# Optimization experiments

Measured on AMD Instinct MI355X. Metric: run time of the kernel, lower is better.

Reference implementation:

```python
import jax, jax.numpy as jnp
import numpy as np

T, N, D, V = 512, 256, 1024, 128000  # total tokens, sampled tokens, d_model, vocab


def setup_inputs() -> dict:
    key = jax.random.key(0)
    k1, k2, k3, k4, k5 = jax.random.split(key, 5)
    hidden_states = jax.random.normal(k1, (T, D), dtype=jnp.float32)
    embedding = jax.random.normal(k2, (V, D), dtype=jnp.float32) * 0.02
    # temperatures in [0.5, 1.5): realistic, avoids divide blow-up (0.0 maps to 1.0 in source)
    temperatures = 0.5 + jax.random.uniform(k3, (N,), dtype=jnp.float32)
    # top_p in [0.5, 1.0)
    top_ps = 0.5 + 0.5 * jax.random.uniform(k4, (N,), dtype=jnp.float32)
    last_token_indices = jnp.sort(jax.random.randint(k5, (N,), 0, T))
    return {
        "hidden_states": hidden_states,
        "embedding": embedding,
        "temperatures": temperatures,
        "top_ps": top_ps,
        "last_token_indices": last_token_indices,
    }


def reference(hidden_states, embedding, temperatures, top_ps, last_token_indices):
    # gather last-token hidden states, project to vocab logits
    h = hidden_states[last_token_indices]              # [N, D]
    logits = jnp.einsum("nd,vd->nv", h, embedding)     # [N, V]
    # temperature softmax
    probs = jax.nn.softmax(logits / temperatures[:, None], axis=-1)
    # top-p: descending sort, cumsum, mask tail, renormalize, un-sort
    order = jnp.argsort(-probs, axis=-1)               # descending order indices
    probs_sort = jnp.take_along_axis(probs, order, axis=-1)
    cum = jnp.cumsum(probs_sort, axis=-1)
    mask = (cum - probs_sort) > top_ps[:, None]
    probs_sort = jnp.where(mask, 0.0, probs_sort)
    probs_sort = probs_sort / jnp.sum(probs_sort, axis=-1, keepdims=True)
    inv = jnp.argsort(order, axis=-1)                  # inverse permutation
    probs_f = jnp.take_along_axis(probs_sort, inv, axis=-1)
    # multinomial sampling (one token per row), fixed key for determinism
    tokens = jax.random.categorical(jax.random.key(42), jnp.log(probs_f + 1e-20), axis=-1)
    return probs_f, tokens
```

## Files before the change

kernel.cpp:

```cpp
#include <hip/hip_runtime.h>
#include <stdint.h>

#define N_TOK 256
#define D_MODEL 1024
#define VOCAB 128000
#define NV_ELEMS (256LL * 128000LL)
#define LIST_CAP 24576
#define GLIST_CAP 16384

typedef unsigned long long u64;
typedef uint32_t u32;
typedef __attribute__((ext_vector_type(8))) short bfrag;
typedef __attribute__((ext_vector_type(4))) float facc;

__device__ __forceinline__ uint32_t bf16_rne_bits(float x) {
    uint32_t u = __float_as_uint(x);
    return (u + 0x7fffu + ((u >> 16) & 1u)) >> 16;
}

__device__ __forceinline__ uint32_t rotl32(uint32_t x, int d) {
    return (x << d) | (x >> (32 - d));
}

__device__ __forceinline__ u32 mono32(u32 b) {
    return (b & 0x80000000u) ? ~b : (b | 0x80000000u);
}
__device__ __forceinline__ float unmono32(u32 k) {
    u32 b = (k & 0x80000000u) ? (k & 0x7FFFFFFFu) : ~k;
    return __uint_as_float(b);
}

__device__ __forceinline__ u64 fixmass(float rv) {
    return (u64)(rv * 1073741824.0f);
}

__device__ __forceinline__ uint2 tf_0_42(uint32_t c0, uint32_t c1) {
    const uint32_t ks0 = 0u, ks1 = 42u, ks2 = 0x1BD11BDAu ^ 42u;
    uint32_t x0 = c0 + ks0, x1 = c1 + ks1;
#define R4(a,b,c,d) \
    x0 += x1; x1 = rotl32(x1,a); x1 ^= x0; \
    x0 += x1; x1 = rotl32(x1,b); x1 ^= x0; \
    x0 += x1; x1 = rotl32(x1,c); x1 ^= x0; \
    x0 += x1; x1 = rotl32(x1,d); x1 ^= x0;
    R4(13,15,26,6)   x0 += ks1; x1 += ks2 + 1u;
    R4(17,29,16,24)  x0 += ks2; x1 += ks0 + 2u;
    R4(13,15,26,6)   x0 += ks0; x1 += ks1 + 3u;
    R4(17,29,16,24)  x0 += ks1; x1 += ks2 + 4u;
    R4(13,15,26,6)   x0 += ks2; x1 += ks0 + 5u;
#undef R4
    return make_uint2(x0, x1);
}

__device__ __forceinline__ uint32_t jax_bits(uint32_t j) {
    uint2 r = tf_0_42(0u, j);
    return r.x ^ r.y;
}

__device__ __forceinline__ float jax_gumbel(uint32_t bits) {
    const float TINY = 1.17549435e-38f;
    float u = __uint_as_float((bits >> 9) | 0x3f800000u) - 1.0f;
    u = u + TINY;
    u = fmaxf(TINY, u);
    return -__logf(-__logf(u));
}

__device__ __forceinline__ float rv_of(float l, float rinv) {
    return __expf(l * rinv);
}

__device__ __forceinline__ void async_copy16(const void* g, void* lbase, int lane) {
#if defined(__has_builtin) && __has_builtin(__builtin_amdgcn_global_load_lds)
    __builtin_amdgcn_global_load_lds((const uint32_t*)g, (uint32_t*)lbase, 16, 0, 0);
#else
    *(bfrag*)((char*)lbase + lane * 16) = *(const bfrag*)g;
#endif
}

__device__ __forceinline__ void scan_desc_u64(const u64* h, int nb, u64 carry, u64 P,
                                              int* outCb, u64* outSa) {
    int lane = (int)threadIdx.x & 63;
    int chunk = nb >> 6;
    int top = nb - 1 - lane * chunk;
    u64 ls = 0ull;
    for (int j = 0; j < chunk; ++j) ls += h[top - j];
    u64 incl = ls;
    for (int o = 1; o < 64; o <<= 1) {
        u64 v = __shfl_up(incl, o, 64);
        if (lane >= o) incl += v;
    }
    u64 s0 = carry + incl - ls;
    unsigned long long mask = __ballot(s0 + ls > P);
    if (mask == 0ull) {
        if (lane == 0) { *outCb = 0; *outSa = carry; }
    } else {
        int cstar = (int)__builtin_ctzll(mask);
        if (lane == cstar) {
            u64 sa = s0; int cb = 0;
            for (int j = 0; j < chunk; ++j) {
                int b = top - j;
                if (sa + h[b] > P) { cb = b; break; }
                sa += h[b];
            }
            *outCb = cb; *outSa = sa;
        }
    }
}

__global__ __launch_bounds__(256) void prep_a(
        const float* __restrict__ hidden, const int* __restrict__ idx,
        ushort* __restrict__ wsA) {
    const int m = blockIdx.x;
    const int t = threadIdx.x;
    const float* src = hidden + (long long)idx[m] * D_MODEL;
    const uint32_t swz = (uint32_t)((m & 7) << 4);
    for (int j = 0; j < 4; ++j) {
        int k = t * 4 + j;
        float x = src[k];
        uint32_t hb = bf16_rne_bits(x);
        float hf = __uint_as_float(hb << 16);
        uint32_t lb = bf16_rne_bits(x - hf);
        int kt = k >> 5, kk = k & 31, g = kk >> 3, e = kk & 7;
        char* img = (char*)wsA + (size_t)kt * 32768;
        uint32_t base = (uint32_t)(m * 128 + g * 32);
        *(ushort*)(img + ((base + 0) ^ swz) + e * 2) = (ushort)hb;
        *(ushort*)(img + ((base + 16) ^ swz) + e * 2) = (ushort)lb;
    }
}

__global__ __launch_bounds__(256) void gemm_mfma(
        const ushort* __restrict__ wsA, const float* __restrict__ emb,
        float* __restrict__ logits) {
    __shared__ __align__(16) ushort Aimg[16384];
    __shared__ __align__(16) ushort Bimg[4096];
    const int tid = (int)threadIdx.x;
    const int w = tid >> 6, l = tid & 63;
    const int lr = l & 15, lg = l >> 4;
    const int v0 = blockIdx.x * 64;
    char* Ab = (char*)Aimg;
    char* Bb = (char*)Bimg;

    facc acc[4][4] = {};

    for (int kt = 0; kt < 32; ++kt) {
        __syncthreads();
        const char* asrc = (const char*)wsA + (size_t)kt * 32768;
#pragma unroll
        for (int i = 0; i < 8; ++i) {
            int off = w * 8192 + i * 1024;
            async_copy16(asrc + off + l * 16, Ab + off, l);
        }
        {
            int rb = tid >> 2, g = tid & 3;
            const float* bs = emb + (size_t)(v0 + rb) * D_MODEL + kt * 32 + g * 8;
            float4 x0 = *(const float4*)bs;
            float4 x1 = *(const float4*)(bs + 4);
            float xs[8] = {x0.x, x0.y, x0.z, x0.w, x1.x, x1.y, x1.z, x1.w};
            bfrag h, lo;
#pragma unroll
            for (int e = 0; e < 8; ++e) {
                uint32_t hb = bf16_rne_bits(xs[e]);
                float hf = __uint_as_float(hb << 16);
                uint32_t lb = bf16_rne_bits(xs[e] - hf);
                h[e] = (short)hb; lo[e] = (short)lb;
            }
            uint32_t swz = (uint32_t)((rb & 7) << 4);
            uint32_t base = (uint32_t)(rb * 128 + g * 32);
            *(bfrag*)(Bb + ((base + 0) ^ swz)) = h;
            *(bfrag*)(Bb + ((base + 16) ^ swz)) = lo;
        }
        __syncthreads();
        bfrag bh[4], bl[4];
#pragma unroll
        for (int nj = 0; nj < 4; ++nj) {
            int rb = nj * 16 + lr;
            uint32_t swz = (uint32_t)((rb & 7) << 4);
            uint32_t base = (uint32_t)(rb * 128 + lg * 32);
            bh[nj] = *(const bfrag*)(Bb + ((base + 0) ^ swz));
            bl[nj] = *(const bfrag*)(Bb + ((base + 16) ^ swz));
        }
#pragma unroll
        for (int mi = 0; mi < 4; ++mi) {
            int r = w * 64 + mi * 16 + lr;
            uint32_t swz = (uint32_t)((r & 7) << 4);
            uint32_t base = (uint32_t)(r * 128 + lg * 32);
            bfrag ah = *(const bfrag*)(Ab + ((base + 0) ^ swz));
            bfrag al = *(const bfrag*)(Ab + ((base + 16) ^ swz));
#pragma unroll
            for (int nj = 0; nj < 4; ++nj) {
                acc[mi][nj] = __builtin_amdgcn_mfma_f32_16x16x32_bf16(ah, bh[nj], acc[mi][nj], 0, 0, 0);
                acc[mi][nj] = __builtin_amdgcn_mfma_f32_16x16x32_bf16(ah, bl[nj], acc[mi][nj], 0, 0, 0);
                acc[mi][nj] = __builtin_amdgcn_mfma_f32_16x16x32_bf16(al, bh[nj], acc[mi][nj], 0, 0, 0);
            }
        }
    }
#pragma unroll
    for (int mi = 0; mi < 4; ++mi) {
        int mbase = w * 64 + mi * 16 + lg * 4;
#pragma unroll
        for (int nj = 0; nj < 4; ++nj) {
            int v = v0 + nj * 16 + lr;
#pragma unroll
            for (int reg = 0; reg < 4; ++reg)
                logits[(size_t)(mbase + reg) * VOCAB + v] = acc[mi][nj][reg];
        }
    }
}

__global__ __launch_bounds__(256) void gemm_kernel(
        const float* __restrict__ hidden, const int* __restrict__ idx,
        const float* __restrict__ emb, float* __restrict__ logits) {
    __shared__ float As[16][64];
    __shared__ float Bs[16][64];
    const int n0 = blockIdx.x * 64, v0 = blockIdx.y * 64;
    const int tid = threadIdx.x;
    const int tx = tid & 15, ty = tid >> 4;
    const int lr = tid >> 2, lk = (tid & 3) * 4;
    float acc[4][4] = {};
    const long long aRow = (long long)idx[n0 + lr] * D_MODEL + lk;
    const long long bRow = (long long)(v0 + lr) * D_MODEL + lk;
    for (int k0 = 0; k0 < D_MODEL; k0 += 16) {
        float4 av = *(const float4*)(hidden + aRow + k0);
        float4 bv = *(const float4*)(emb + bRow + k0);
        __syncthreads();
        As[lk + 0][lr] = av.x; As[lk + 1][lr] = av.y; As[lk + 2][lr] = av.z; As[lk + 3][lr] = av.w;
        Bs[lk + 0][lr] = bv.x; Bs[lk + 1][lr] = bv.y; Bs[lk + 2][lr] = bv.z; Bs[lk + 3][lr] = bv.w;
        __syncthreads();
#pragma unroll
        for (int kk = 0; kk < 16; ++kk) {
            float4 a = *(const float4*)&As[kk][ty * 4];
            float4 b = *(const float4*)&Bs[kk][tx * 4];
            float aa[4] = {a.x, a.y, a.z, a.w};
            float bb[4] = {b.x, b.y, b.z, b.w};
#pragma unroll
            for (int i = 0; i < 4; ++i)
#pragma unroll
                for (int j = 0; j < 4; ++j)
                    acc[i][j] += aa[i] * bb[j];
        }
    }
#pragma unroll
    for (int i = 0; i < 4; ++i) {
        float4 o = make_float4(acc[i][0], acc[i][1], acc[i][2], acc[i][3]);
        *(float4*)(logits + (long long)(n0 + ty * 4 + i) * VOCAB + (v0 + tx * 4)) = o;
    }
}

__global__ __launch_bounds__(512) void hist1_kernel(
        const float* __restrict__ probs, const float* __restrict__ temps,
        u64* __restrict__ ghist) {
    const int row = blockIdx.y, hb = blockIdx.x, tid = (int)threadIdx.x;
    __shared__ u64 h[4096];
    for (int i = tid; i < 4096; i += 512) h[i] = 0ull;
    __syncthreads();
    const float rinv = 1.0f / temps[row];
    const float4* R4 = (const float4*)(probs + (size_t)row * VOCAB);
    const int base4 = hb * 8000;
    for (int i = 0; i < 16; ++i) {
        int j = tid + i * 512;
        if (j < 8000) {
            float4 x = R4[base4 + j];
            float xs[4] = {x.x, x.y, x.z, x.w};
#pragma unroll
            for (int c = 0; c < 4; ++c) {
                u32 key = mono32(__float_as_uint(xs[c]));
                atomicAdd(&h[key >> 20], fixmass(rv_of(xs[c], rinv)));
            }
        }
    }
    __syncthreads();
    u64* gh = ghist + (size_t)row * 4096;
    for (int i = tid; i < 4096; i += 512)
        if (h[i]) atomicAdd(&gh[i], h[i]);
}

__global__ __launch_bounds__(64) void scan1_kernel(
        const u64* __restrict__ ghist, const float* __restrict__ topps,
        u64* __restrict__ rsP, u64* __restrict__ rsCarry, u32* __restrict__ rsCb) {
    const int row = blockIdx.x, lane = (int)threadIdx.x;
    const u64* h = ghist + (size_t)row * 4096;
    u64 S = 0ull;
    for (int j = lane; j < 4096; j += 64) S += h[j];
    for (int o = 32; o >= 1; o >>= 1) S += __shfl_xor(S, o, 64);
    const u64 P = (u64)((double)topps[row] * (double)S);
    __shared__ int sCb; __shared__ u64 sSa;
    scan_desc_u64(h, 4096, 0ull, P, &sCb, &sSa);
    __syncthreads();
    if (lane == 0) { rsP[row] = P; rsCarry[row] = sSa; rsCb[row] = (u32)sCb; }
}

__global__ __launch_bounds__(512) void compact_kernel(
        const float* __restrict__ probs, const u32* __restrict__ rsCb,
        u64* __restrict__ list, u32* __restrict__ listCnt) {
    const int row = blockIdx.y, hb = blockIdx.x, tid = (int)threadIdx.x;
    __shared__ u64 buf[4096];
    __shared__ u32 lcnt, gbase;
    const u32 cb1 = rsCb[row];
    const float4* R4 = (const float4*)(probs + (size_t)row * VOCAB);
    u64* lst = list + (size_t)row * GLIST_CAP;
    const int base4 = hb * 8000;
    if (tid == 0) lcnt = 0u;
    __syncthreads();
    for (int pair = 0; pair < 8; ++pair) {
#pragma unroll
        for (int s = 0; s < 2; ++s) {
            int j = tid + (pair * 2 + s) * 512;
            if (j < 8000) {
                float4 x = R4[base4 + j];
                float xs[4] = {x.x, x.y, x.z, x.w};
#pragma unroll
                for (int c = 0; c < 4; ++c) {
                    u32 key = mono32(__float_as_uint(xs[c]));
                    if ((key >> 20) == cb1) {
                        u32 pos = atomicAdd(&lcnt, 1u);
                        buf[pos] = ((u64)key << 32) | (u32)((base4 + j) * 4 + c);
                    }
                }
            }
        }
        __syncthreads();
        u32 n = lcnt;
        if (n) {
            if (tid == 0) gbase = atomicAdd(&listCnt[row], n);
            __syncthreads();
            u32 gb = gbase;
            for (u32 i2 = tid; i2 < n; i2 += 512) {
                u32 gpos = gb + i2;
                if (gpos < GLIST_CAP) lst[gpos] = buf[i2];
            }
        }
        __syncthreads();
        if (tid == 0) lcnt = 0u;
        __syncthreads();
    }
}

__global__ __launch_bounds__(1024) void resolve_kernel(
        const u64* __restrict__ list, const u32* __restrict__ listCnt,
        const u64* __restrict__ rsP, const u64* __restrict__ rsCarry,
        const u32* __restrict__ rsCb, const float* __restrict__ temps,
        u32* __restrict__ scTs, u32* __restrict__ scTieN,
        float* __restrict__ scInvSp, u32* __restrict__ tieKept) {
    const int row = blockIdx.x, tid = (int)threadIdx.x;
    __shared__ u64 h2[1024];
    __shared__ u32 c3[1024];
    __shared__ int sCb; __shared__ u64 sSa;
    __shared__ u32 sTc;
    __shared__ u32 tlist[1024];
    const u32 cnt = min(listCnt[row], (u32)GLIST_CAP);
    const u64 P = rsP[row];
    const float rinv = 1.0f / temps[row];
    const u64* lst = list + (size_t)row * GLIST_CAP;

    h2[tid] = 0ull;
    __syncthreads();
    for (u32 j = tid; j < cnt; j += 1024) {
        u32 key = (u32)(lst[j] >> 32);
        atomicAdd(&h2[(key >> 10) & 1023u], fixmass(rv_of(unmono32(key), rinv)));
    }
    __syncthreads();
    if (tid < 64) scan_desc_u64(h2, 1024, rsCarry[row], P, &sCb, &sSa);
    __syncthreads();
    const u32 cb2 = (u32)sCb; const u64 carry2 = sSa;
    __syncthreads();

    h2[tid] = 0ull; c3[tid] = 0u;
    __syncthreads();
    for (u32 j = tid; j < cnt; j += 1024) {
        u32 key = (u32)(lst[j] >> 32);
        if (((key >> 10) & 1023u) == cb2) {
            atomicAdd(&h2[key & 1023u], fixmass(rv_of(unmono32(key), rinv)));
            atomicAdd(&c3[key & 1023u], 1u);
        }
    }
    __syncthreads();
    if (tid < 64) scan_desc_u64(h2, 1024, carry2, P, &sCb, &sSa);
    __syncthreads();
    const int cb3 = sCb; const u64 sa3 = sSa;
    const u32 ts = (rsCb[row] << 20) | (cb2 << 10) | (u32)cb3;
    u32 cntb = c3[cb3]; if (cntb == 0u) cntb = 1u;
    const u64 tfq = fixmass(rv_of(unmono32(ts), rinv));
    const u64 rem = P - sa3;
    u32 mt;
    if (tfq == 0ull) mt = cntb;
    else {
        u64 q = rem / tfq;
        mt = (q >= (u64)(cntb - 1)) ? cntb : ((u32)q + 1u);
    }
    const u64 Spq = sa3 + (u64)mt * tfq;

    if (tid == 0) sTc = 0u;
    __syncthreads();
    for (u32 j = tid; j < cnt; j += 1024) {
        if ((u32)(lst[j] >> 32) == ts) {
            u32 pos = atomicAdd(&sTc, 1u);
            if (pos < 1024u) tlist[pos] = (u32)lst[j];
        }
    }
    __syncthreads();
    const u32 tn = min(sTc, 1024u);
    if ((u32)tid < tn) {
        u32 my = tlist[tid];
        u32 rank = 0;
        for (u32 j2 = 0; j2 < tn; ++j2) rank += (tlist[j2] < my) ? 1u : 0u;
        if (rank < mt) tieKept[(size_t)row * 1024 + rank] = my;
    }
    if (tid == 0) {
        scTs[row] = ts;
        scTieN[row] = min(mt, tn);
        scInvSp[row] = (float)(1073741824.0 / (double)Spq);
    }
}

__global__ __launch_bounds__(512) void final2_kernel(
        float* __restrict__ probs, const float* __restrict__ temps,
        const u32* __restrict__ scTs, const u32* __restrict__ scTieN,
        const float* __restrict__ scInvSp, const u32* __restrict__ tieKept,
        u64* __restrict__ argmax) {
    const int row = blockIdx.y, hb = blockIdx.x, tid = (int)threadIdx.x;
    __shared__ u32 tl[1024];
    __shared__ u64 wbest[8];
    const u32 ts = scTs[row], tieN = scTieN[row];
    const float invSp = scInvSp[row];
    const float rinv = 1.0f / temps[row];
    for (u32 i = tid; i < tieN; i += 512) tl[i] = tieKept[(size_t)row * 1024 + i];
    __syncthreads();
    float4* R4 = (float4*)(probs + (size_t)row * VOCAB);
    const u32 rowBase = (u32)row * (u32)VOCAB;
    const int base4 = hb * 8000;
    u64 best = 0ull;
    for (int i = 0; i < 16; ++i) {
        int j = tid + i * 512;
        if (j < 8000) {
            float4 x = R4[base4 + j];
            float xs[4] = {x.x, x.y, x.z, x.w};
            float4 out;
            float* op = (float*)&out;
#pragma unroll
            for (int c = 0; c < 4; ++c) {
                u32 key = mono32(__float_as_uint(xs[c]));
                u32 v = (u32)((base4 + j) * 4 + c);
                bool kept = key > ts;
                if (key == ts) {
                    kept = false;
                    for (u32 q2 = 0; q2 < tieN; ++q2)
                        if (tl[q2] == v) { kept = true; break; }
                }
                if (kept) {
                    float pf = rv_of(xs[c], rinv) * invSp;
                    op[c] = pf;
                    float g = jax_gumbel(jax_bits(rowBase + v));
                    float val = __logf(pf + 1e-20f) + g;
                    u64 pk = ((u64)mono32(__float_as_uint(val)) << 32) | (u32)(~v);
                    if (pk > best) best = pk;
                } else {
                    op[c] = 0.0f;
                }
            }
            R4[base4 + j] = out;
        }
    }
    for (int o = 32; o >= 1; o >>= 1) {
        u64 ob = __shfl_xor(best, o, 64);
        if (ob > best) best = ob;
    }
    if ((tid & 63) == 0) wbest[tid >> 6] = best;
    __syncthreads();
    if (tid == 0) {
        u64 b = wbest[0];
        for (int w2 = 1; w2 < 8; ++w2) if (wbest[w2] > b) b = wbest[w2];
        atomicMax(&argmax[row], b);
    }
}

__global__ void token_kernel(const u64* __restrict__ argmax, float* __restrict__ outTok) {
    int n = (int)threadIdx.x;
    if (n < N_TOK) outTok[n] = (float)(~(u32)argmax[n]);
}

__device__ __forceinline__ void scan_desc_wave(const float* h, int nb, float carry,
                                               float P, int* outCb, float* outSa) {
    int lane = (int)threadIdx.x & 63;
    int chunk = nb >> 6;
    int top = nb - 1 - lane * chunk;
    float ls = 0.0f;
    for (int j = 0; j < chunk; ++j) ls += h[top - j];
    float incl = ls;
    for (int o = 1; o < 64; o <<= 1) {
        float v = __shfl_up(incl, o, 64);
        if (lane >= o) incl += v;
    }
    float s0 = carry + incl - ls;
    unsigned long long mask = __ballot(s0 + ls > P);
    if (mask == 0ull) {
        if (lane == 63) { *outCb = 0; *outSa = carry + incl - h[0]; }
    } else {
        int cstar = (int)__builtin_ctzll(mask);
        if (lane == cstar) {
            float sa = s0; int cb = 0;
            for (int j = 0; j < chunk; ++j) {
                int b = top - j;
                if (sa + h[b] > P) { cb = b; break; }
                sa += h[b];
            }
            *outCb = cb; *outSa = sa;
        }
    }
}

__global__ __launch_bounds__(1024) void sample_kernel(
        float* __restrict__ probs, const float* __restrict__ temps,
        const float* __restrict__ topps, float* __restrict__ outTok) {
    const int row = blockIdx.x;
    const int tid = (int)threadIdx.x;
    float* L = probs + (long long)row * VOCAB;
    const float4* L4 = (const float4*)L;
    float4* L4w = (float4*)L;

    __shared__ float waveH[16][2048];
    __shared__ float hsum[2048];
    __shared__ uint32_t hcnt[1024];
    __shared__ float wred[16];
    __shared__ float aVal[16];
    __shared__ int aIdx[16];
    __shared__ uint32_t tieList[256];
    __shared__ int sCb;
    __shared__ float sSa;
    __shared__ float sP, sCarry1, sCarry2, sSp, sInvSp;
    __shared__ uint32_t sPref1, sCb2, sTsKey, sMt, sTieN, sCnt;
    uint32_t* keys = (uint32_t*)&waveH[4][0];

    const float t = temps[row];
    const float p = topps[row];
    const float rinv = 1.0f / t;

    for (int i = tid; i < 16 * 2048; i += 1024) ((float*)waveH)[i] = 0.0f;
    __syncthreads();
    {
        float* myH = waveH[tid >> 6];
#pragma unroll 2
        for (int i = 0; i < 31; ++i) {
            float4 x = L4[tid + i * 1024];
            float r0 = rv_of(x.x, rinv), r1 = rv_of(x.y, rinv);
            float r2 = rv_of(x.z, rinv), r3 = rv_of(x.w, rinv);
            atomicAdd(&myH[__float_as_uint(r0) >> 20], r0);
            atomicAdd(&myH[__float_as_uint(r1) >> 20], r1);
            atomicAdd(&myH[__float_as_uint(r2) >> 20], r2);
            atomicAdd(&myH[__float_as_uint(r3) >> 20], r3);
        }
        if (tid < 256) {
            float4 x = L4[31744 + tid];
            float r0 = rv_of(x.x, rinv), r1 = rv_of(x.y, rinv);
            float r2 = rv_of(x.z, rinv), r3 = rv_of(x.w, rinv);
            atomicAdd(&myH[__float_as_uint(r0) >> 20], r0);
            atomicAdd(&myH[__float_as_uint(r1) >> 20], r1);
            atomicAdd(&myH[__float_as_uint(r2) >> 20], r2);
            atomicAdd(&myH[__float_as_uint(r3) >> 20], r3);
        }
    }
    __syncthreads();
    {
        float a0 = 0.0f, a1 = 0.0f;
#pragma unroll
        for (int w2 = 0; w2 < 16; ++w2) { a0 += waveH[w2][tid]; a1 += waveH[w2][tid + 1024]; }
        hsum[tid] = a0; hsum[tid + 1024] = a1;
        float s = a0 + a1;
        for (int o = 32; o >= 1; o >>= 1) s += __shfl_xor(s, o, 64);
        if ((tid & 63) == 0) wred[tid >> 6] = s;
    }
    __syncthreads();
    if (tid == 0) {
        float tot = 0.0f;
        for (int w2 = 0; w2 < 16; ++w2) tot += wred[w2];
        sP = p * tot;
    }
    __syncthreads();
    if (tid < 64) scan_desc_wave(hsum, 2048, 0.0f, sP, &sCb, &sSa);
    __syncthreads();
    if (tid == 0) { sPref1 = (uint32_t)sCb; sCarry1 = sSa; sCnt = 0u; }
    __syncthreads();

    const uint32_t pref1 = sPref1;
    const float P = sP;
#pragma unroll 2
    for (int i = 0; i < 31; ++i) {
        float4 x = L4[tid + i * 1024];
        float rr[4] = {rv_of(x.x, rinv), rv_of(x.y, rinv), rv_of(x.z, rinv), rv_of(x.w, rinv)};
#pragma unroll
        for (int c = 0; c < 4; ++c) {
            uint32_t key = __float_as_uint(rr[c]);
            if ((key >> 20) == pref1) {
                uint32_t pos = atomicAdd(&sCnt, 1u);
                if (pos < LIST_CAP) keys[pos] = key;
            }
        }
    }
    if (tid < 256) {
        float4 x = L4[31744 + tid];
        float rr[4] = {rv_of(x.x, rinv), rv_of(x.y, rinv), rv_of(x.z, rinv), rv_of(x.w, rinv)};
#pragma unroll
        for (int c = 0; c < 4; ++c) {
            uint32_t key = __float_as_uint(rr[c]);
            if ((key >> 20) == pref1) {
                uint32_t pos = atomicAdd(&sCnt, 1u);
                if (pos < LIST_CAP) keys[pos] = key;
            }
        }
    }
    __syncthreads();
    const uint32_t K = sCnt;
    const bool inLds = (K <= LIST_CAP);

    if (tid < 1024) hsum[tid] = 0.0f;
    __syncthreads();
    if (inLds) {
        for (uint32_t j = tid; j < K; j += 1024) {
            uint32_t key = keys[j];
            atomicAdd(&hsum[(key >> 10) & 1023u], __uint_as_float(key));
        }
    } else {
        for (int i = 0; i < 125; ++i) {
            int v = tid + i * 1024;
            float rv = rv_of(L[v], rinv);
            uint32_t key = __float_as_uint(rv);
            if ((key >> 20) == pref1) atomicAdd(&hsum[(key >> 10) & 1023u], rv);
        }
    }
    __syncthreads();
    if (tid < 64) scan_desc_wave(hsum, 1024, sCarry1, P, &sCb, &sSa);
    __syncthreads();
    if (tid == 0) { sCb2 = (uint32_t)sCb; sCarry2 = sSa; }
    __syncthreads();

    const uint32_t cb2 = sCb2;
    if (tid < 1024) { hsum[tid] = 0.0f; hcnt[tid] = 0u; }
    __syncthreads();
    if (inLds) {
        for (uint32_t j = tid; j < K; j += 1024) {
            uint32_t key = keys[j];
            if (((key >> 10) & 1023u) == cb2) {
                atomicAdd(&hsum[key & 1023u], __uint_as_float(key));
                atomicAdd(&hcnt[key & 1023u], 1u);
            }
        }
    } else {
        const uint32_t pref2full = (pref1 << 10) | cb2;
        for (int i = 0; i < 125; ++i) {
            int v = tid + i * 1024;
            float rv = rv_of(L[v], rinv);
            uint32_t key = __float_as_uint(rv);
            if ((key >> 10) == pref2full) {
                atomicAdd(&hsum[key & 1023u], rv);
                atomicAdd(&hcnt[key & 1023u], 1u);
            }
        }
    }
    __syncthreads();
    if (tid < 64) scan_desc_wave(hsum, 1024, sCarry2, P, &sCb, &sSa);
    __syncthreads();
    if (tid == 0) {
        int cb3 = sCb; float sa3 = sSa;
        uint32_t ts = (pref1 << 20) | (cb2 << 10) | (uint32_t)cb3;
        uint32_t cnt = hcnt[cb3]; if (cnt == 0u) cnt = 1u;
        float tf = __uint_as_float(ts);
        uint32_t mt;
        float rem = P - sa3; if (rem < 0.0f) rem = 0.0f;
        if (!(tf > 0.0f)) mt = cnt;
        else {
            float q = floorf(rem / tf);
            mt = (q >= (float)(cnt - 1)) ? cnt : ((uint32_t)q + 1u);
        }
        sTsKey = ts; sMt = mt;
        sSp = sa3 + (float)mt * tf;
        sInvSp = 1.0f / sSp;
        sTieN = 0u;
    }
    __syncthreads();

    const uint32_t ts = sTsKey, mt = sMt;
    const float invSp = sInvSp;
    float bestV = -INFINITY;
    int bestI = 0x7FFFFFFF;
    const uint32_t rowBase = (uint32_t)row * (uint32_t)VOCAB;
    for (int i = 0; i < 32; ++i) {
        int f4i = (i < 31) ? (tid + i * 1024) : (31744 + tid);
        if (i == 31 && tid >= 256) break;
        float4 x = L4[f4i];
        float rr[4] = {rv_of(x.x, rinv), rv_of(x.y, rinv), rv_of(x.z, rinv), rv_of(x.w, rinv)};
        float4 out;
        float* op = (float*)&out;
#pragma unroll
        for (int c = 0; c < 4; ++c) {
            uint32_t key = __float_as_uint(rr[c]);
            int v = f4i * 4 + c;
            if (key > ts) {
                float pf = rr[c] * invSp;
                op[c] = pf;
                float g = jax_gumbel(jax_bits(rowBase + (uint32_t)v));
                float val = __logf(pf + 1e-20f) + g;
                if (val > bestV || (val == bestV && v < bestI)) { bestV = val; bestI = v; }
            } else if (key == ts) {
                op[c] = 0.0f;
                uint32_t pos = atomicAdd(&sTieN, 1u);
                if (pos < 256u) tieList[pos] = (uint32_t)v;
            } else {
                op[c] = 0.0f;
            }
        }
        L4w[f4i] = out;
    }
    __syncthreads();
    {
        const uint32_t tn = min(sTieN, 256u);
        if ((uint32_t)tid < tn) {
            uint32_t v = tieList[tid];
            uint32_t rank = 0;
            for (uint32_t j = 0; j < tn; ++j) rank += (tieList[j] < v) ? 1u : 0u;
            if (rank < mt) {
                float pf = __uint_as_float(ts) * invSp;
                L[v] = pf;
                float g = jax_gumbel(jax_bits(rowBase + v));
                float val = __logf(pf + 1e-20f) + g;
                if (val > bestV || (val == bestV && (int)v < bestI)) { bestV = val; bestI = (int)v; }
            }
        }
    }
    for (int o = 32; o >= 1; o >>= 1) {
        float ov = __shfl_xor(bestV, o, 64);
        int oi = __shfl_xor(bestI, o, 64);
        if (ov > bestV || (ov == bestV && oi < bestI)) { bestV = ov; bestI = oi; }
    }
    if ((tid & 63) == 0) { aVal[tid >> 6] = bestV; aIdx[tid >> 6] = bestI; }
    __syncthreads();
    if (tid == 0) {
        float bv = aVal[0]; int bi = aIdx[0];
        for (int w2 = 1; w2 < 16; ++w2) {
            if (aVal[w2] > bv || (aVal[w2] == bv && aIdx[w2] < bi)) { bv = aVal[w2]; bi = aIdx[w2]; }
        }
        outTok[row] = (float)bi;
    }
}

extern "C" void kernel_launch(void* const* d_in, const int* in_sizes, int n_in,
                              void* d_out, int out_size, void* d_ws, size_t ws_size,
                              hipStream_t stream) {
    const float* hidden = (const float*)d_in[0];
    const float* emb    = (const float*)d_in[1];
    const float* temps  = (const float*)d_in[2];
    const float* topps  = (const float*)d_in[3];
    const int*   idx    = (const int*)d_in[4];

    float* probs  = (float*)d_out;
    float* outTok = probs + NV_ELEMS;

    char* ws = (char*)d_ws;
    const bool wsGemm = ws_size >= (size_t)(1u << 20);
    const bool wsBig  = ws_size >= (size_t)(44u << 20);

    if (wsBig) {
        u64* ghist   = (u64*)(ws + (1u << 20));
        char* m      = ws + (41u << 20);
        hipMemsetAsync(ghist, 0, (size_t)256 * 4096 * 8, stream);
        hipMemsetAsync(m, 0, 1024, stream);
        hipMemsetAsync(m + 9216, 0, 2048, stream);
    }

    if (wsGemm) {
        ushort* wsA = (ushort*)ws;
        prep_a<<<N_TOK, 256, 0, stream>>>(hidden, idx, wsA);
        gemm_mfma<<<VOCAB / 64, 256, 0, stream>>>(wsA, emb, probs);
    } else {
        gemm_kernel<<<dim3(4, 2000), 256, 0, stream>>>(hidden, idx, emb, probs);
    }

    if (wsBig) {
        u64* ghist     = (u64*)(ws + (1u << 20));
        u64* list      = (u64*)(ws + (9u << 20));
        char* m        = ws + (41u << 20);
        u32* listCnt   = (u32*)(m);
        u32* rsCb      = (u32*)(m + 1024);
        u64* rsP       = (u64*)(m + 2048);
        u64* rsCarry   = (u64*)(m + 4096);
        u32* scTs      = (u32*)(m + 6144);
        u32* scTieN    = (u32*)(m + 7168);
        float* scInvSp = (float*)(m + 8192);
        u64* argmax    = (u64*)(m + 9216);
        u32* tieKept   = (u32*)(m + 16384);

        hist1_kernel<<<dim3(4, N_TOK), 512, 0, stream>>>(probs, temps, ghist);
        scan1_kernel<<<N_TOK, 64, 0, stream>>>(ghist, topps, rsP, rsCarry, rsCb);
        compact_kernel<<<dim3(4, N_TOK), 512, 0, stream>>>(probs, rsCb, list, listCnt);
        resolve_kernel<<<N_TOK, 1024, 0, stream>>>(list, listCnt, rsP, rsCarry, rsCb,
                                                   temps, scTs, scTieN, scInvSp, tieKept);
        final2_kernel<<<dim3(4, N_TOK), 512, 0, stream>>>(probs, temps, scTs, scTieN,
                                                          scInvSp, tieKept, argmax);
        token_kernel<<<1, 256, 0, stream>>>(argmax, outTok);
    } else {
        sample_kernel<<<N_TOK, 1024, 0, stream>>>(probs, temps, topps, outTok);
    }
}
```

Before: 449.3 us.

## Drop histogram memsets and atomics using per-block partial histograms

Each hist1 block now writes its 4096-bin histogram to its own slot in the list buffer instead of atomically adding into a zeroed global histogram. scan1 sums the four partials into shared memory before scanning, and it also zeroes listCnt and argmax. That removes all three hipMemsetAsync calls and the global atomics. GLIST_CAP grows and the workspace threshold rises to 280 MB, so if the workspace is smaller the code falls back to the slow single-kernel sampler.

Result: faster. 439.3 us (-2.2%).

```diff
diff --git a/kernel.cpp b/kernel.cpp
--- a/kernel.cpp
+++ b/kernel.cpp
@@ -6,7 +6,7 @@
 #define VOCAB 128000
 #define NV_ELEMS (256LL * 128000LL)
 #define LIST_CAP 24576
-#define GLIST_CAP 16384
+#define GLIST_CAP 131072
 
 typedef unsigned long long u64;
 typedef uint32_t u32;
@@ -247,7 +247,7 @@
 
 __global__ __launch_bounds__(512) void hist1_kernel(
         const float* __restrict__ probs, const float* __restrict__ temps,
-        u64* __restrict__ ghist) {
+        u64* __restrict__ hpart) {
     const int row = blockIdx.y, hb = blockIdx.x, tid = (int)threadIdx.x;
     __shared__ u64 h[4096];
     for (int i = tid; i < 4096; i += 512) h[i] = 0ull;
@@ -268,24 +268,33 @@
         }
     }
     __syncthreads();
-    u64* gh = ghist + (size_t)row * 4096;
-    for (int i = tid; i < 4096; i += 512)
-        if (h[i]) atomicAdd(&gh[i], h[i]);
+    u64* gh = hpart + ((size_t)row * 4 + hb) * 4096;
+    for (int i = tid; i < 4096; i += 512) gh[i] = h[i];
 }
 
 __global__ __launch_bounds__(64) void scan1_kernel(
-        const u64* __restrict__ ghist, const float* __restrict__ topps,
-        u64* __restrict__ rsP, u64* __restrict__ rsCarry, u32* __restrict__ rsCb) {
+        const u64* __restrict__ hpart, const float* __restrict__ topps,
+        u64* __restrict__ rsP, u64* __restrict__ rsCarry, u32* __restrict__ rsCb,
+        u32* __restrict__ listCnt, u64* __restrict__ argmax) {
     const int row = blockIdx.x, lane = (int)threadIdx.x;
-    const u64* h = ghist + (size_t)row * 4096;
+    __shared__ u64 sh[4096];
+    const u64* hp = hpart + (size_t)row * 4 * 4096;
     u64 S = 0ull;
-    for (int j = lane; j < 4096; j += 64) S += h[j];
+    for (int j = lane; j < 4096; j += 64) {
+        u64 v = hp[j] + hp[4096 + j] + hp[8192 + j] + hp[12288 + j];
+        sh[j] = v;
+        S += v;
+    }
+    __syncthreads();
     for (int o = 32; o >= 1; o >>= 1) S += __shfl_xor(S, o, 64);
     const u64 P = (u64)((double)topps[row] * (double)S);
     __shared__ int sCb; __shared__ u64 sSa;
-    scan_desc_u64(h, 4096, 0ull, P, &sCb, &sSa);
-    __syncthreads();
-    if (lane == 0) { rsP[row] = P; rsCarry[row] = sSa; rsCb[row] = (u32)sCb; }
+    scan_desc_u64(sh, 4096, 0ull, P, &sCb, &sSa);
+    __syncthreads();
+    if (lane == 0) {
+        rsP[row] = P; rsCarry[row] = sSa; rsCb[row] = (u32)sCb;
+        listCnt[row] = 0u; argmax[row] = 0ull;
+    }
 }
 
 __global__ __launch_bounds__(512) void compact_kernel(
@@ -754,15 +763,7 @@
 
     char* ws = (char*)d_ws;
     const bool wsGemm = ws_size >= (size_t)(1u << 20);
-    const bool wsBig  = ws_size >= (size_t)(44u << 20);
-
-    if (wsBig) {
-        u64* ghist   = (u64*)(ws + (1u << 20));
-        char* m      = ws + (41u << 20);
-        hipMemsetAsync(ghist, 0, (size_t)256 * 4096 * 8, stream);
-        hipMemsetAsync(m, 0, 1024, stream);
-        hipMemsetAsync(m + 9216, 0, 2048, stream);
-    }
+    const bool wsBig  = ws_size >= (size_t)(280u << 20);
 
     if (wsGemm) {
         ushort* wsA = (ushort*)ws;
@@ -773,9 +774,8 @@
     }
 
     if (wsBig) {
-        u64* ghist     = (u64*)(ws + (1u << 20));
-        u64* list      = (u64*)(ws + (9u << 20));
-        char* m        = ws + (41u << 20);
+        u64* list      = (u64*)(ws + (2u << 20));
+        char* m        = ws + (2u << 20) + ((size_t)256u << 20);
         u32* listCnt   = (u32*)(m);
         u32* rsCb      = (u32*)(m + 1024);
         u64* rsP       = (u64*)(m + 2048);
@@ -786,8 +786,9 @@
         u64* argmax    = (u64*)(m + 9216);
         u32* tieKept   = (u32*)(m + 16384);
 
-        hist1_kernel<<<dim3(4, N_TOK), 512, 0, stream>>>(probs, temps, ghist);
-        scan1_kernel<<<N_TOK, 64, 0, stream>>>(ghist, topps, rsP, rsCarry, rsCb);
+        hist1_kernel<<<dim3(4, N_TOK), 512, 0, stream>>>(probs, temps, list);
+        scan1_kernel<<<N_TOK, 64, 0, stream>>>(list, topps, rsP, rsCarry, rsCb,
+                                               listCnt, argmax);
         compact_kernel<<<dim3(4, N_TOK), 512, 0, stream>>>(probs, rsCb, list, listCnt);
         resolve_kernel<<<N_TOK, 1024, 0, stream>>>(list, listCnt, rsP, rsCarry, rsCb,
                                                    temps, scTs, scTieN, scInvSp, tieKept);
```

## Fuse top-p histogram, scan, compact and resolve into one per-row kernel

Applied to the files above, without the earlier changes.

Replaces the four-kernel top-p threshold pipeline (global histogram, scan, compaction into a global list, resolve) with a single 1024-thread block per row. The block rebuilds the three radix-level histograms by re-reading the row from memory three or four times instead of compacting candidates. This drops the memsets, global atomics, list writes and several launches. It also adds a fast path that skips tie listing when every tied element is kept. The cost is only 256 blocks for the whole job and repeated full-row reads per block, which may leave parallelism on the table compared with the 4-way split per row.

Result: faster. 434.0 us (-3.4%).

```diff
diff --git a/kernel.cpp b/kernel.cpp
--- a/kernel.cpp
+++ b/kernel.cpp
@@ -6,7 +6,7 @@
 #define VOCAB 128000
 #define NV_ELEMS (256LL * 128000LL)
 #define LIST_CAP 24576
-#define GLIST_CAP 16384
+#define TIE_ALL 0xFFFFFFFFu
 
 typedef unsigned long long u64;
 typedef uint32_t u32;
@@ -245,169 +245,152 @@
     }
 }
 
-__global__ __launch_bounds__(512) void hist1_kernel(
+__global__ __launch_bounds__(1024) void resolveC_kernel(
         const float* __restrict__ probs, const float* __restrict__ temps,
-        u64* __restrict__ ghist) {
-    const int row = blockIdx.y, hb = blockIdx.x, tid = (int)threadIdx.x;
-    __shared__ u64 h[4096];
-    for (int i = tid; i < 4096; i += 512) h[i] = 0ull;
-    __syncthreads();
+        const float* __restrict__ topps,
+        u32* __restrict__ scTs, u32* __restrict__ scTieN,
+        float* __restrict__ scInvSp, u32* __restrict__ tieKept,
+        u64* __restrict__ argmax) {
+    const int row = blockIdx.x, tid = (int)threadIdx.x;
+    __shared__ u64 h1[4096];
+    __shared__ u32 c3[1024];
+    __shared__ u32 tlist[1024];
+    __shared__ u64 wredu[16];
+    __shared__ int sCb; __shared__ u64 sSa;
+    __shared__ u64 sP;
+    __shared__ u32 sTc, sTsKey, sMt, sCntb;
+    __shared__ float sInv;
+
     const float rinv = 1.0f / temps[row];
     const float4* R4 = (const float4*)(probs + (size_t)row * VOCAB);
-    const int base4 = hb * 8000;
-    for (int i = 0; i < 16; ++i) {
-        int j = tid + i * 512;
-        if (j < 8000) {
-            float4 x = R4[base4 + j];
+
+    for (int i = tid; i < 4096; i += 1024) h1[i] = 0ull;
+    __syncthreads();
+    for (int i = 0; i < 32; ++i) {
+        int j = tid + i * 1024;
+        if (j < 32000) {
+            float4 x = R4[j];
             float xs[4] = {x.x, x.y, x.z, x.w};
 #pragma unroll
             for (int c = 0; c < 4; ++c) {
                 u32 key = mono32(__float_as_uint(xs[c]));
-                atomicAdd(&h[key >> 20], fixmass(rv_of(xs[c], rinv)));
-            }
-        }
-    }
-    __syncthreads();
-    u64* gh = ghist + (size_t)row * 4096;
-    for (int i = tid; i < 4096; i += 512)
-        if (h[i]) atomicAdd(&gh[i], h[i]);
-}
-
-__global__ __launch_bounds__(64) void scan1_kernel(
-        const u64* __restrict__ ghist, const float* __restrict__ topps,
-        u64* __restrict__ rsP, u64* __restrict__ rsCarry, u32* __restrict__ rsCb) {
-    const int row = blockIdx.x, lane = (int)threadIdx.x;
-    const u64* h = ghist + (size_t)row * 4096;
-    u64 S = 0ull;
-    for (int j = lane; j < 4096; j += 64) S += h[j];
-    for (int o = 32; o >= 1; o >>= 1) S += __shfl_xor(S, o, 64);
-    const u64 P = (u64)((double)topps[row] * (double)S);
-    __shared__ int sCb; __shared__ u64 sSa;
-    scan_desc_u64(h, 4096, 0ull, P, &sCb, &sSa);
-    __syncthreads();
-    if (lane == 0) { rsP[row] = P; rsCarry[row] = sSa; rsCb[row] = (u32)sCb; }
-}
-
-__global__ __launch_bounds__(512) void compact_kernel(
-        const float* __restrict__ probs, const u32* __restrict__ rsCb,
-        u64* __restrict__ list, u32* __restrict__ listCnt) {
-    const int row = blockIdx.y, hb = blockIdx.x, tid = (int)threadIdx.x;
-    __shared__ u64 buf[4096];
-    __shared__ u32 lcnt, gbase;
-    const u32 cb1 = rsCb[row];
-    const float4* R4 = (const float4*)(probs + (size_t)row * VOCAB);
-    u64* lst = list + (size_t)row * GLIST_CAP;
-    const int base4 = hb * 8000;
-    if (tid == 0) lcnt = 0u;
-    __syncthreads();
-    for (int pair = 0; pair < 8; ++pair) {
-#pragma unroll
-        for (int s = 0; s < 2; ++s) {
-            int j = tid + (pair * 2 + s) * 512;
-            if (j < 8000) {
-                float4 x = R4[base4 + j];
+                atomicAdd(&h1[key >> 20], fixmass(rv_of(xs[c], rinv)));
+            }
+        }
+    }
+    __syncthreads();
+    {
+        u64 s = h1[tid] + h1[tid + 1024] + h1[tid + 2048] + h1[tid + 3072];
+        for (int o = 32; o >= 1; o >>= 1) s += __shfl_xor(s, o, 64);
+        if ((tid & 63) == 0) wredu[tid >> 6] = s;
+    }
+    __syncthreads();
+    if (tid == 0) {
+        u64 S = 0ull;
+        for (int w2 = 0; w2 < 16; ++w2) S += wredu[w2];
+        sP = (u64)((double)topps[row] * (double)S);
+    }
+    __syncthreads();
+    const u64 P = sP;
+    if (tid < 64) scan_desc_u64(h1, 4096, 0ull, P, &sCb, &sSa);
+    __syncthreads();
+    const u32 cb1 = (u32)sCb; const u64 carry1 = sSa;
+    __syncthreads();
+
+    h1[tid] = 0ull;
+    __syncthreads();
+    for (int i = 0; i < 32; ++i) {
+        int j = tid + i * 1024;
+        if (j < 32000) {
+            float4 x = R4[j];
+            float xs[4] = {x.x, x.y, x.z, x.w};
+#pragma unroll
+            for (int c = 0; c < 4; ++c) {
+                u32 key = mono32(__float_as_uint(xs[c]));
+                if ((key >> 20) == cb1)
+                    atomicAdd(&h1[(key >> 10) & 1023u], fixmass(rv_of(xs[c], rinv)));
+            }
+        }
+    }
+    __syncthreads();
+    if (tid < 64) scan_desc_u64(h1, 1024, carry1, P, &sCb, &sSa);
+    __syncthreads();
+    const u32 cb2 = (u32)sCb; const u64 carry2 = sSa;
+    __syncthreads();
+
+    const u32 pref2 = (cb1 << 10) | cb2;
+    h1[tid] = 0ull; c3[tid] = 0u;
+    __syncthreads();
+    for (int i = 0; i < 32; ++i) {
+        int j = tid + i * 1024;
+        if (j < 32000) {
+            float4 x = R4[j];
+            float xs[4] = {x.x, x.y, x.z, x.w};
+#pragma unroll
+            for (int c = 0; c < 4; ++c) {
+                u32 key = mono32(__float_as_uint(xs[c]));
+                if ((key >> 10) == pref2) {
+                    atomicAdd(&h1[key & 1023u], fixmass(rv_of(xs[c], rinv)));
+                    atomicAdd(&c3[key & 1023u], 1u);
+                }
+            }
+        }
+    }
+    __syncthreads();
+    if (tid < 64) scan_desc_u64(h1, 1024, carry2, P, &sCb, &sSa);
+    __syncthreads();
+    if (tid == 0) {
+        const int cb3 = sCb; const u64 sa3 = sSa;
+        u32 ts = (pref2 << 10) | (u32)cb3;
+        u32 cntb = c3[cb3]; if (cntb == 0u) cntb = 1u;
+        u64 tfq = fixmass(rv_of(unmono32(ts), rinv));
+        u64 rem = P - sa3;
+        u32 mt;
+        if (tfq == 0ull) mt = cntb;
+        else {
+            u64 q = rem / tfq;
+            mt = (q >= (u64)(cntb - 1)) ? cntb : ((u32)q + 1u);
+        }
+        u64 Spq = sa3 + (u64)mt * tfq;
+        sTsKey = ts; sMt = mt; sCntb = cntb;
+        sInv = (float)(1073741824.0 / (double)Spq);
+        sTc = 0u;
+    }
+    __syncthreads();
+    const u32 ts = sTsKey, mt = sMt, cntb = sCntb;
+
+    if (mt < cntb) {
+        for (int i = 0; i < 32; ++i) {
+            int j = tid + i * 1024;
+            if (j < 32000) {
+                float4 x = R4[j];
                 float xs[4] = {x.x, x.y, x.z, x.w};
 #pragma unroll
                 for (int c = 0; c < 4; ++c) {
                     u32 key = mono32(__float_as_uint(xs[c]));
-                    if ((key >> 20) == cb1) {
-                        u32 pos = atomicAdd(&lcnt, 1u);
-                        buf[pos] = ((u64)key << 32) | (u32)((base4 + j) * 4 + c);
+                    if (key == ts) {
+                        u32 pos = atomicAdd(&sTc, 1u);
+                        if (pos < 1024u) tlist[pos] = (u32)(j * 4 + c);
                     }
                 }
             }
         }
         __syncthreads();
-        u32 n = lcnt;
-        if (n) {
-            if (tid == 0) gbase = atomicAdd(&listCnt[row], n);
-            __syncthreads();
-            u32 gb = gbase;
-            for (u32 i2 = tid; i2 < n; i2 += 512) {
-                u32 gpos = gb + i2;
-                if (gpos < GLIST_CAP) lst[gpos] = buf[i2];
-            }
-        }
-        __syncthreads();
-        if (tid == 0) lcnt = 0u;
-        __syncthreads();
-    }
-}
-
-__global__ __launch_bounds__(1024) void resolve_kernel(
-        const u64* __restrict__ list, const u32* __restrict__ listCnt,
-        const u64* __restrict__ rsP, const u64* __restrict__ rsCarry,
-        const u32* __restrict__ rsCb, const float* __restrict__ temps,
-        u32* __restrict__ scTs, u32* __restrict__ scTieN,
-        float* __restrict__ scInvSp, u32* __restrict__ tieKept) {
-    const int row = blockIdx.x, tid = (int)threadIdx.x;
-    __shared__ u64 h2[1024];
-    __shared__ u32 c3[1024];
-    __shared__ int sCb; __shared__ u64 sSa;
-    __shared__ u32 sTc;
-    __shared__ u32 tlist[1024];
-    const u32 cnt = min(listCnt[row], (u32)GLIST_CAP);
-    const u64 P = rsP[row];
-    const float rinv = 1.0f / temps[row];
-    const u64* lst = list + (size_t)row * GLIST_CAP;
-
-    h2[tid] = 0ull;
-    __syncthreads();
-    for (u32 j = tid; j < cnt; j += 1024) {
-        u32 key = (u32)(lst[j] >> 32);
-        atomicAdd(&h2[(key >> 10) & 1023u], fixmass(rv_of(unmono32(key), rinv)));
-    }
-    __syncthreads();
-    if (tid < 64) scan_desc_u64(h2, 1024, rsCarry[row], P, &sCb, &sSa);
-    __syncthreads();
-    const u32 cb2 = (u32)sCb; const u64 carry2 = sSa;
-    __syncthreads();
-
-    h2[tid] = 0ull; c3[tid] = 0u;
-    __syncthreads();
-    for (u32 j = tid; j < cnt; j += 1024) {
-        u32 key = (u32)(lst[j] >> 32);
-        if (((key >> 10) & 1023u) == cb2) {
-            atomicAdd(&h2[key & 1023u], fixmass(rv_of(unmono32(key), rinv)));
-            atomicAdd(&c3[key & 1023u], 1u);
-        }
-    }
-    __syncthreads();
-    if (tid < 64) scan_desc_u64(h2, 1024, carry2, P, &sCb, &sSa);
-    __syncthreads();
-    const int cb3 = sCb; const u64 sa3 = sSa;
-    const u32 ts = (rsCb[row] << 20) | (cb2 << 10) | (u32)cb3;
-    u32 cntb = c3[cb3]; if (cntb == 0u) cntb = 1u;
-    const u64 tfq = fixmass(rv_of(unmono32(ts), rinv));
-    const u64 rem = P - sa3;
-    u32 mt;
-    if (tfq == 0ull) mt = cntb;
-    else {
-        u64 q = rem / tfq;
-        mt = (q >= (u64)(cntb - 1)) ? cntb : ((u32)q + 1u);
-    }
-    const u64 Spq = sa3 + (u64)mt * tfq;
-
-    if (tid == 0) sTc = 0u;
-    __syncthreads();
-    for (u32 j = tid; j < cnt; j += 1024) {
-        if ((u32)(lst[j] >> 32) == ts) {
-            u32 pos = atomicAdd(&sTc, 1u);
-            if (pos < 1024u) tlist[pos] = (u32)lst[j];
-        }
-    }
-    __syncthreads();
-    const u32 tn = min(sTc, 1024u);
-    if ((u32)tid < tn) {
-        u32 my = tlist[tid];
-        u32 rank = 0;
-        for (u32 j2 = 0; j2 < tn; ++j2) rank += (tlist[j2] < my) ? 1u : 0u;
-        if (rank < mt) tieKept[(size_t)row * 1024 + rank] = my;
+        const u32 tn = min(sTc, 1024u);
+        if ((u32)tid < tn) {
+            u32 my = tlist[tid];
+            u32 rank = 0;
+            for (u32 j2 = 0; j2 < tn; ++j2) rank += (tlist[j2] < my) ? 1u : 0u;
+            if (rank < mt) tieKept[(size_t)row * 1024 + rank] = my;
+        }
+        if (tid == 0) scTieN[row] = min(mt, tn);
+    } else {
+        if (tid == 0) scTieN[row] = TIE_ALL;
     }
     if (tid == 0) {
         scTs[row] = ts;
-        scTieN[row] = min(mt, tn);
-        scInvSp[row] = (float)(1073741824.0 / (double)Spq);
+        scInvSp[row] = sInv;
+        argmax[row] = 0ull;
     }
 }
 
@@ -420,9 +403,10 @@
     __shared__ u32 tl[1024];
     __shared__ u64 wbest[8];
     const u32 ts = scTs[row], tieN = scTieN[row];
+    const u32 tlN = (tieN == TIE_ALL) ? 0u : tieN;
     const float invSp = scInvSp[row];
     const float rinv = 1.0f / temps[row];
-    for (u32 i = tid; i < tieN; i += 512) tl[i] = tieKept[(size_t)row * 1024 + i];
+    for (u32 i = tid; i < tlN; i += 512) tl[i] = tieKept[(size_t)row * 1024 + i];
     __syncthreads();
     float4* R4 = (float4*)(probs + (size_t)row * VOCAB);
     const u32 rowBase = (u32)row * (u32)VOCAB;
@@ -441,9 +425,13 @@
                 u32 v = (u32)((base4 + j) * 4 + c);
                 bool kept = key > ts;
                 if (key == ts) {
-                    kept = false;
-                    for (u32 q2 = 0; q2 < tieN; ++q2)
-                        if (tl[q2] == v) { kept = true; break; }
+                    if (tieN == TIE_ALL) {
+                        kept = true;
+                    } else {
+                        kept = false;
+                        for (u32 q2 = 0; q2 < tlN; ++q2)
+                            if (tl[q2] == v) { kept = true; break; }
+                    }
                 }
                 if (kept) {
                     float pf = rv_of(xs[c], rinv) * invSp;
@@ -754,15 +742,7 @@
 
     char* ws = (char*)d_ws;
     const bool wsGemm = ws_size >= (size_t)(1u << 20);
-    const bool wsBig  = ws_size >= (size_t)(44u << 20);
-
-    if (wsBig) {
-        u64* ghist   = (u64*)(ws + (1u << 20));
-        char* m      = ws + (41u << 20);
-        hipMemsetAsync(ghist, 0, (size_t)256 * 4096 * 8, stream);
-        hipMemsetAsync(m, 0, 1024, stream);
-        hipMemsetAsync(m + 9216, 0, 2048, stream);
-    }
+    const bool wsBig  = ws_size >= (size_t)(4u << 20);
 
     if (wsGemm) {
         ushort* wsA = (ushort*)ws;
@@ -773,24 +753,16 @@
     }
 
     if (wsBig) {
-        u64* ghist     = (u64*)(ws + (1u << 20));
-        u64* list      = (u64*)(ws + (9u << 20));
-        char* m        = ws + (41u << 20);
-        u32* listCnt   = (u32*)(m);
-        u32* rsCb      = (u32*)(m + 1024);
-        u64* rsP       = (u64*)(m + 2048);
-        u64* rsCarry   = (u64*)(m + 4096);
-        u32* scTs      = (u32*)(m + 6144);
-        u32* scTieN    = (u32*)(m + 7168);
-        float* scInvSp = (float*)(m + 8192);
-        u64* argmax    = (u64*)(m + 9216);
-        u32* tieKept   = (u32*)(m + 16384);
-
-        hist1_kernel<<<dim3(4, N_TOK), 512, 0, stream>>>(probs, temps, ghist);
-        scan1_kernel<<<N_TOK, 64, 0, stream>>>(ghist, topps, rsP, rsCarry, rsCb);
-        compact_kernel<<<dim3(4, N_TOK), 512, 0, stream>>>(probs, rsCb, list, listCnt);
-        resolve_kernel<<<N_TOK, 1024, 0, stream>>>(list, listCnt, rsP, rsCarry, rsCb,
-                                                   temps, scTs, scTieN, scInvSp, tieKept);
+        char* m        = ws + (2u << 20);
+        u32* scTs      = (u32*)(m);
+        u32* scTieN    = (u32*)(m + 1024);
+        float* scInvSp = (float*)(m + 2048);
+        u64* argmax    = (u64*)(m + 3072);
+        u32* tieKept   = (u32*)(m + 8192);
+
+        resolveC_kernel<<<N_TOK, 1024, 0, stream>>>(probs, temps, topps,
+                                                    scTs, scTieN, scInvSp,
+                                                    tieKept, argmax);
         final2_kernel<<<dim3(4, N_TOK), 512, 0, stream>>>(probs, temps, scTs, scTieN,
                                                           scInvSp, tieKept, argmax);
         token_kernel<<<1, 256, 0, stream>>>(argmax, outTok);
```
